# Optimization experiments

Measured on AMD Instinct MI355X. Metric: run time of the kernel, lower is better.

## Reference

```python
import jax, jax.numpy as jnp
import numpy as np

VQ_NUM = 3
EMB_NUM = 1024
COMMITMENT_WEIGHT = 1.0
# cumprod of [1, emb_num, emb_num] -> per-stage index bases
CUMPROD = [1, EMB_NUM, EMB_NUM * EMB_NUM]


def setup_inputs() -> dict:
    key = jax.random.key(0)
    k0, k1, k2, k3 = jax.random.split(key, 4)
    z = jax.random.normal(k0, (8, 4096, 512), dtype=jnp.float32)
    # linear_in: nn.Linear(in_ch=512, emb_ch=256, bias=False) -> weight [emb_ch, in_ch]
    W_in = jax.random.normal(k1, (VQ_NUM, 256, 512), dtype=jnp.float32) * 0.02
    # linear_out: nn.Linear(emb_ch=256, in_ch=512, bias=False) -> weight [in_ch, emb_ch]
    W_out = jax.random.normal(k2, (VQ_NUM, 512, 256), dtype=jnp.float32) * 0.02
    # one codebook per stage (share_residual_codebooks=False)
    codebooks = jax.random.normal(k3, (VQ_NUM, EMB_NUM, 256), dtype=jnp.float32) * 0.02
    return {"z": z, "W_in": W_in, "W_out": W_out, "codebooks": codebooks}


def reference(z, W_in, W_out, codebooks):
    sg = jax.lax.stop_gradient
    z_q = jnp.zeros_like(z)
    r = z
    loss = jnp.float32(0.0)
    index_sum = jnp.zeros(z.shape[:2], dtype=jnp.int64 if jax.config.jax_enable_x64 else jnp.int32)
    for i in range(VQ_NUM):
        # linear_in
        zi = jnp.einsum('bnc,ec->bne', r, W_in[i])  # [B,N,emb_ch]
        v = codebooks[i]  # [S, emb_ch]
        # squared L2 distance: ||z||^2 + ||v||^2 - 2 z.v
        dist = (jnp.sum(zi * zi, axis=-1, keepdims=True)
                + jnp.sum(v * v, axis=-1)
                - 2.0 * jnp.einsum('bne,se->bns', zi, v))  # [B,N,S]
        idx = jnp.argmin(dist, axis=-1)  # [B,N] int
        zq = v[idx]  # codebook lookup, [B,N,emb_ch]
        loss = loss + (COMMITMENT_WEIGHT * jnp.mean((sg(zq) - zi) ** 2)
                       + jnp.mean((zq - sg(zi)) ** 2))
        # straight-through estimator
        zq_ste = zi + sg(zq - zi)
        # linear_out
        r_q = jnp.einsum('bne,ce->bnc', zq_ste, W_out[i])  # [B,N,in_ch]
        index_sum = index_sum + idx.astype(index_sum.dtype) * CUMPROD[i]
        z_q = z_q + r_q
        r = z - sg(z_q)
    loss = loss / VQ_NUM + jnp.mean((z_q - z) ** 2)
    return z_q, index_sum, loss
```

## Files before the change

kernel.cpp:

```cpp
#include <hip/hip_runtime.h>

#define MTOK 32768
#define CIN  512
#define EMB  256
#define NCODE 1024
#define VQ   3
#define DELTA 2e-3f

typedef short s16x8 __attribute__((ext_vector_type(8)));
typedef float f32x4 __attribute__((ext_vector_type(4)));
typedef unsigned short u16;

static __device__ __forceinline__ u16 f2bf(float x) {
    unsigned int u = __float_as_uint(x);
    u += 0x7FFF + ((u >> 16) & 1);
    return (u16)(u >> 16);
}
static __device__ __forceinline__ float bf2f(u16 h) {
    return __uint_as_float(((unsigned int)h) << 16);
}

__global__ void init_k(double* loss_acc, int* cnt) {
    loss_acc[0] = 0.0;
    loss_acc[1] = 0.0;
    cnt[0] = 0; cnt[1] = 0; cnt[2] = 0;
}

__global__ __launch_bounds__(64) void prep_cb_k(const float* __restrict__ cbs,
                                                double* __restrict__ vnorm64,
                                                float* __restrict__ vnorm32,
                                                u16* __restrict__ cbh,
                                                u16* __restrict__ cbl) {
    int s = blockIdx.x;
    const float* row = cbs + (size_t)s * EMB;
    double acc = 0.0;
    for (int k = threadIdx.x; k < EMB; k += 64) {
        float v = row[k];
        double vd = (double)v; acc += vd * vd;
        u16 h = f2bf(v);
        u16 l = f2bf(v - bf2f(h));
        cbh[(size_t)s * EMB + k] = h;
        cbl[(size_t)s * EMB + k] = l;
    }
    #pragma unroll
    for (int off = 32; off > 0; off >>= 1) acc += __shfl_down(acc, off, 64);
    if (threadIdx.x == 0) { vnorm64[s] = acc; vnorm32[s] = (float)acc; }
}

__global__ __launch_bounds__(256) void prep_w_k(const float* __restrict__ W_in,
                                                u16* __restrict__ wh,
                                                u16* __restrict__ wl) {
    int i = blockIdx.x * 256 + threadIdx.x;
    float v = W_in[i];
    u16 h = f2bf(v);
    wh[i] = h;
    wl[i] = f2bf(v - bf2f(h));
}

__global__ __launch_bounds__(256) void prep_wt_k(const float* __restrict__ W_in,
                                                 float* __restrict__ WinT) {
    int i = blockIdx.x * 256 + threadIdx.x;
    int s = i / (EMB * CIN);
    int rem = i - s * (EMB * CIN);
    int e = rem / CIN;
    int k = rem - e * CIN;
    WinT[(size_t)s * CIN * EMB + (size_t)k * EMB + e] = W_in[i];
}

__global__ __launch_bounds__(256) void prep_T_k(const float* __restrict__ cbs,
                                                const float* __restrict__ Wout,
                                                float* __restrict__ T) {
    const int stage = blockIdx.z;
    const float* A = cbs  + (size_t)stage * NCODE * EMB;
    const float* B = Wout + (size_t)stage * CIN * EMB;
    float* C = T + (size_t)stage * NCODE * CIN;
    __shared__ float As[64][33];
    __shared__ float Bs[64][33];
    const int tid = threadIdx.x;
    const int ty = tid >> 4, tx = tid & 15;
    const int m0 = blockIdx.x * 64;
    const int n0 = blockIdx.y * 64;
    const int lrow = tid >> 5, lcol = tid & 31;
    double acc[4][4];
    #pragma unroll
    for (int i = 0; i < 4; ++i)
        #pragma unroll
        for (int j = 0; j < 4; ++j) acc[i][j] = 0.0;

    for (int k0 = 0; k0 < EMB; k0 += 32) {
        __syncthreads();
        #pragma unroll
        for (int t = 0; t < 8; ++t) {
            int r = lrow + 8 * t;
            As[r][lcol] = A[(size_t)(m0 + r) * EMB + k0 + lcol];
            Bs[r][lcol] = B[(size_t)(n0 + r) * EMB + k0 + lcol];
        }
        __syncthreads();
        #pragma unroll
        for (int k = 0; k < 32; ++k) {
            double a[4], b[4];
            #pragma unroll
            for (int i = 0; i < 4; ++i) a[i] = (double)As[ty * 4 + i][k];
            #pragma unroll
            for (int j = 0; j < 4; ++j) b[j] = (double)Bs[tx * 4 + j][k];
            #pragma unroll
            for (int i = 0; i < 4; ++i)
                #pragma unroll
                for (int j = 0; j < 4; ++j) acc[i][j] += a[i] * b[j];
        }
    }
    #pragma unroll
    for (int i = 0; i < 4; ++i) {
        float4 v = make_float4((float)acc[i][0], (float)acc[i][1],
                               (float)acc[i][2], (float)acc[i][3]);
        *reinterpret_cast<float4*>(&C[(size_t)(m0 + ty * 4 + i) * CIN + n0 + tx * 4]) = v;
    }
}

__global__ __launch_bounds__(256, 2) void zi_mfma_k(const float* __restrict__ z,
                                                    const float* __restrict__ zq,
                                                    const u16* __restrict__ wh,
                                                    const u16* __restrict__ wl,
                                                    float* __restrict__ zi,
                                                    double* __restrict__ loss_acc,
                                                    int stage0) {
    __shared__ __align__(16) u16 swh[2][16][520];
    __shared__ __align__(16) u16 swl[2][16][520];
    const int tid = threadIdx.x;
    const int w = tid >> 6;
    const int l = tid & 63;
    const int col = l & 15;
    const int g = l >> 4;
    const int mw = blockIdx.x * 64 + w * 16;
    const int sr = tid >> 4, sq = tid & 15;

    s16x8 ah[16], al[16];
    {
        const float* zr = z  + (size_t)(mw + col) * CIN + g * 8;
        const float* qr = zq + (size_t)(mw + col) * CIN + g * 8;
        #pragma unroll
        for (int kc = 0; kc < 16; ++kc) {
            float4 f0 = *reinterpret_cast<const float4*>(zr + kc * 32);
            float4 f1 = *reinterpret_cast<const float4*>(zr + kc * 32 + 4);
            float f[8] = {f0.x, f0.y, f0.z, f0.w, f1.x, f1.y, f1.z, f1.w};
            if (!stage0) {
                float4 q0 = *reinterpret_cast<const float4*>(qr + kc * 32);
                float4 q1 = *reinterpret_cast<const float4*>(qr + kc * 32 + 4);
                f[0] -= q0.x; f[1] -= q0.y; f[2] -= q0.z; f[3] -= q0.w;
                f[4] -= q1.x; f[5] -= q1.y; f[6] -= q1.z; f[7] -= q1.w;
            }
            #pragma unroll
            for (int j = 0; j < 8; ++j) {
                u16 h = f2bf(f[j]);
                u16 lo = f2bf(f[j] - bf2f(h));
                ah[kc][j] = (short)h; al[kc][j] = (short)lo;
            }
        }
    }

    const u16* gh = wh + (size_t)sr * CIN + sq * 8;
    const u16* gl = wl + (size_t)sr * CIN + sq * 8;
    uint4 h0, h1, h2, h3, l0, l1, l2, l3;
#define ZLOAD(NT) do { const u16* th = gh + (size_t)(NT) * (16 * CIN);                \
    const u16* tl = gl + (size_t)(NT) * (16 * CIN);                                   \
    h0 = *(const uint4*)(th);        h1 = *(const uint4*)(th + 128);                  \
    h2 = *(const uint4*)(th + 256);  h3 = *(const uint4*)(th + 384);                  \
    l0 = *(const uint4*)(tl);        l1 = *(const uint4*)(tl + 128);                  \
    l2 = *(const uint4*)(tl + 256);  l3 = *(const uint4*)(tl + 384); } while (0)
#define ZWRITE(P) do {                                                                \
    *(uint4*)&swh[P][sr][sq * 8]       = h0;  *(uint4*)&swh[P][sr][sq * 8 + 128] = h1;\
    *(uint4*)&swh[P][sr][sq * 8 + 256] = h2;  *(uint4*)&swh[P][sr][sq * 8 + 384] = h3;\
    *(uint4*)&swl[P][sr][sq * 8]       = l0;  *(uint4*)&swl[P][sr][sq * 8 + 128] = l1;\
    *(uint4*)&swl[P][sr][sq * 8 + 256] = l2;  *(uint4*)&swl[P][sr][sq * 8 + 384] = l3;\
    } while (0)
    ZLOAD(0); ZWRITE(0); ZLOAD(1);

    double zn = 0.0;
    for (int nt = 0; nt < 16; ++nt) {
        __syncthreads();
        const int p = nt & 1;
        if (nt + 1 < 16) ZWRITE((nt + 1) & 1);
        if (nt + 2 < 16) ZLOAD(nt + 2);
        f32x4 a0 = {0.f, 0.f, 0.f, 0.f};
        f32x4 a1 = {0.f, 0.f, 0.f, 0.f};
        f32x4 a2 = {0.f, 0.f, 0.f, 0.f};
        #pragma unroll
        for (int kc = 0; kc < 16; ++kc) {
            s16x8 Bh = *(const s16x8*)&swh[p][col][g * 8 + kc * 32];
            s16x8 Bl = *(const s16x8*)&swl[p][col][g * 8 + kc * 32];
            a0 = __builtin_amdgcn_mfma_f32_16x16x32_bf16(ah[kc], Bh, a0, 0, 0, 0);
            a1 = __builtin_amdgcn_mfma_f32_16x16x32_bf16(al[kc], Bh, a1, 0, 0, 0);
            a2 = __builtin_amdgcn_mfma_f32_16x16x32_bf16(ah[kc], Bl, a2, 0, 0, 0);
        }
        #pragma unroll
        for (int r = 0; r < 4; ++r) {
            float v = a0[r] + a1[r] + a2[r];
            zi[(size_t)(mw + g * 4 + r) * EMB + nt * 16 + col] = v;
            zn += (double)v * (double)v;
        }
    }
#undef ZLOAD
#undef ZWRITE
    #pragma unroll
    for (int off = 32; off > 0; off >>= 1) zn += __shfl_down(zn, off, 64);
    if (l == 0) atomicAdd(loss_acc, zn);
}

__global__ __launch_bounds__(256, 2) void pref_k(const float* __restrict__ zi,
                                                 const u16* __restrict__ cbh,
                                                 const u16* __restrict__ cbl,
                                                 const float* __restrict__ vnorm32,
                                                 int* __restrict__ idx,
                                                 int* __restrict__ idx_sum,
                                                 float* __restrict__ mind,
                                                 int* __restrict__ flagged,
                                                 int* __restrict__ cnt,
                                                 int* __restrict__ cand2,
                                                 double* __restrict__ loss_acc,
                                                 int stage0, int cumprod) {
    __shared__ __align__(16) u16 sbh[2][16][264];
    __shared__ __align__(16) u16 sbl[2][16][264];
    __shared__ double loss_s[16];
    const int tid = threadIdx.x;
    const int w = tid >> 6;
    const int l = tid & 63;
    const int col = l & 15;
    const int g = l >> 4;
    const int mw = blockIdx.x * 64 + w * 16;
    const int sr = tid >> 4, sq = tid & 15;

    s16x8 ah[8], al[8];
    {
        const float* zr = zi + (size_t)(mw + col) * EMB + g * 8;
        #pragma unroll
        for (int kc = 0; kc < 8; ++kc) {
            float4 f0 = *reinterpret_cast<const float4*>(zr + kc * 32);
            float4 f1 = *reinterpret_cast<const float4*>(zr + kc * 32 + 4);
            float f[8] = {f0.x, f0.y, f0.z, f0.w, f1.x, f1.y, f1.z, f1.w};
            #pragma unroll
            for (int j = 0; j < 8; ++j) {
                u16 h = f2bf(f[j]);
                u16 lo = f2bf(f[j] - bf2f(h));
                ah[kc][j] = (short)h;
                al[kc][j] = (short)lo;
            }
        }
    }

    float b1[4] = {1e30f, 1e30f, 1e30f, 1e30f};
    float b2[4] = {1e30f, 1e30f, 1e30f, 1e30f};
    float b3[4] = {1e30f, 1e30f, 1e30f, 1e30f};
    int   i1[4] = {0, 0, 0, 0};
    int   i2[4] = {0, 0, 0, 0};

    const u16* gh = cbh + (size_t)sr * EMB + sq * 8;
    const u16* gl = cbl + (size_t)sr * EMB + sq * 8;
    uint4 h0, h1, l0, l1;
#define PLOAD(CT) do { const u16* th = gh + (size_t)(CT) * (16 * EMB);                \
    const u16* tl = gl + (size_t)(CT) * (16 * EMB);                                   \
    h0 = *(const uint4*)(th);  h1 = *(const uint4*)(th + 128);                        \
    l0 = *(const uint4*)(tl);  l1 = *(const uint4*)(tl + 128); } while (0)
#define PWRITE(P) do {                                                                \
    *(uint4*)&sbh[P][sr][sq * 8] = h0;  *(uint4*)&sbh[P][sr][sq * 8 + 128] = h1;      \
    *(uint4*)&sbl[P][sr][sq * 8] = l0;  *(uint4*)&sbl[P][sr][sq * 8 + 128] = l1;      \
    } while (0)
    PLOAD(0); PWRITE(0); PLOAD(1);

    for (int ct = 0; ct < 64; ++ct) {
        __syncthreads();
        const int p = ct & 1;
        if (ct + 1 < 64) PWRITE((ct + 1) & 1);
        if (ct + 2 < 64) PLOAD(ct + 2);
        const float vn = vnorm32[ct * 16 + col];
        f32x4 a0 = {0.f, 0.f, 0.f, 0.f};
        f32x4 a1 = {0.f, 0.f, 0.f, 0.f};
        f32x4 a2 = {0.f, 0.f, 0.f, 0.f};
        #pragma unroll
        for (int kc = 0; kc < 8; ++kc) {
            s16x8 Bh = *(const s16x8*)&sbh[p][col][g * 8 + kc * 32];
            s16x8 Bl = *(const s16x8*)&sbl[p][col][g * 8 + kc * 32];
            a0 = __builtin_amdgcn_mfma_f32_16x16x32_bf16(ah[kc], Bh, a0, 0, 0, 0);
            a1 = __builtin_amdgcn_mfma_f32_16x16x32_bf16(al[kc], Bh, a1, 0, 0, 0);
            a2 = __builtin_amdgcn_mfma_f32_16x16x32_bf16(ah[kc], Bl, a2, 0, 0, 0);
        }
        #pragma unroll
        for (int r = 0; r < 4; ++r) {
            float sc = vn - 2.f * (a0[r] + a1[r] + a2[r]);
            int c = ct * 16 + col;
            if (sc < b1[r]) { b3[r] = b2[r]; b2[r] = b1[r]; i2[r] = i1[r]; b1[r] = sc; i1[r] = c; }
            else if (sc < b2[r]) { b3[r] = b2[r]; b2[r] = sc; i2[r] = c; }
            else b3[r] = fminf(b3[r], sc);
        }
    }
#undef PLOAD
#undef PWRITE

    #pragma unroll
    for (int off = 1; off < 16; off <<= 1) {
        #pragma unroll
        for (int r = 0; r < 4; ++r) {
            float c1 = __shfl_xor(b1[r], off, 64);
            int   j1 = __shfl_xor(i1[r], off, 64);
            float c2 = __shfl_xor(b2[r], off, 64);
            int   j2 = __shfl_xor(i2[r], off, 64);
            float c3 = __shfl_xor(b3[r], off, 64);
            float nb1, nb2, nb3; int ni1, ni2;
            if (c1 < b1[r] || (c1 == b1[r] && j1 < i1[r])) {
                nb1 = c1; ni1 = j1;
                if (b1[r] < c2 || (b1[r] == c2 && i1[r] < j2)) {
                    nb2 = b1[r]; ni2 = i1[r]; nb3 = fminf(b2[r], c2);
                } else {
                    nb2 = c2; ni2 = j2; nb3 = fminf(b1[r], c3);
                }
            } else {
                nb1 = b1[r]; ni1 = i1[r];
                if (c1 < b2[r] || (c1 == b2[r] && j1 < i2[r])) {
                    nb2 = c1; ni2 = j1; nb3 = fminf(b2[r], c2);
                } else {
                    nb2 = b2[r]; ni2 = i2[r]; nb3 = fminf(c1, b3[r]);
                }
            }
            b1[r] = nb1; b2[r] = nb2; b3[r] = nb3; i1[r] = ni1; i2[r] = ni2;
        }
    }
    if (col == 0) {
        double lsum = 0.0;
        #pragma unroll
        for (int r = 0; r < 4; ++r) {
            int m = mw + g * 4 + r;
            idx[m] = i1[r];
            if (stage0) idx_sum[m] = i1[r];
            else        idx_sum[m] += i1[r] * cumprod;
            mind[m] = b1[r];
            lsum += (double)b1[r];
            if (b2[r] - b1[r] < DELTA) {
                int slot = atomicAdd(cnt, 1);
                int full = (b3[r] - b1[r] < DELTA) ? 1 : 0;
                flagged[slot] = (m << 1) | full;
                cand2[m] = i2[r];
            }
        }
        loss_s[w * 4 + g] = lsum;
    }
    __syncthreads();
    if (tid == 0) {
        double s = 0.0;
        #pragma unroll
        for (int q = 0; q < 16; ++q) s += loss_s[q];
        atomicAdd(loss_acc, s);
    }
}

__global__ __launch_bounds__(256) void rescan_k(const float* __restrict__ z,
                                                const float* __restrict__ zqv,
                                                const float* __restrict__ WinT,
                                                const float* __restrict__ cb,
                                                const double* __restrict__ vnorm64,
                                                const int* __restrict__ flagged,
                                                const int* __restrict__ cnt,
                                                const int* __restrict__ cand2,
                                                int* __restrict__ idx,
                                                int* __restrict__ idx_sum,
                                                float* __restrict__ mind,
                                                double* __restrict__ loss_acc,
                                                int cumprod, int stage0) {
    __shared__ double r64[8][CIN];
    __shared__ int mArr[8], fArr[8], cAArr[8], cBArr[8];
    __shared__ double sredS[4];
    __shared__ int iredS[4];
    double* zi_l = &r64[0][0];
    const int tid = threadIdx.x;
    const int w = tid >> 6, l = tid & 63;
    const int n = *cnt;

    for (int jb = blockIdx.x; jb * 8 < n; jb += gridDim.x) {
        const int nt = min(8, n - jb * 8);
        __syncthreads();
        if (tid < nt) {
            int fm = flagged[jb * 8 + tid];
            int m = fm >> 1;
            mArr[tid] = m; fArr[tid] = fm & 1;
            cAArr[tid] = idx[m]; cBArr[tid] = cand2[m];
        }
        __syncthreads();
        for (int t = 0; t < nt; ++t) {
            const int m = mArr[t];
            #pragma unroll
            for (int h = 0; h < 2; ++h) {
                int k = tid + h * 256;
                float rv = z[(size_t)m * CIN + k];
                if (!stage0) rv -= zqv[(size_t)m * CIN + k];
                r64[t][k] = (double)rv;
            }
        }
        __syncthreads();
        double acc[8] = {0, 0, 0, 0, 0, 0, 0, 0};
        #pragma unroll 4
        for (int k = 0; k < CIN; ++k) {
            double wv = (double)WinT[(size_t)k * EMB + tid];
            #pragma unroll
            for (int t = 0; t < 8; ++t) acc[t] += r64[t][k] * wv;
        }
        __syncthreads();
        #pragma unroll
        for (int t = 0; t < 8; ++t) zi_l[t * 256 + tid] = acc[t];
        __syncthreads();

        for (int t = w; t < nt; t += 4) {
            if (fArr[t]) continue;
            const int cA = cAArr[t], cB = cBArr[t], m = mArr[t];
            const double* zt = zi_l + t * 256;
            float4 vA = *(const float4*)(cb + (size_t)cA * EMB + 4 * l);
            float4 vB = *(const float4*)(cb + (size_t)cB * EMB + 4 * l);
            double z0 = zt[4 * l], z1 = zt[4 * l + 1];
            double z2 = zt[4 * l + 2], z3 = zt[4 * l + 3];
            double sA = z0 * (double)vA.x + z1 * (double)vA.y
                      + z2 * (double)vA.z + z3 * (double)vA.w;
            double sB = z0 * (double)vB.x + z1 * (double)vB.y
                      + z2 * (double)vB.z + z3 * (double)vB.w;
            #pragma unroll
            for (int off = 1; off < 64; off <<= 1) {
                sA += __shfl_xor(sA, off, 64);
                sB += __shfl_xor(sB, off, 64);
            }
            if (l == 0) {
                double dA = vnorm64[cA] - 2.0 * sA;
                double dB = vnorm64[cB] - 2.0 * sB;
                int bi; double best;
                if (dB < dA || (dB == dA && cB < cA)) { bi = cB; best = dB; }
                else                                   { bi = cA; best = dA; }
                int oldI = idx[m];
                if (bi != oldI) { idx[m] = bi; idx_sum[m] += (bi - oldI) * cumprod; }
                atomicAdd(loss_acc, best - (double)mind[m]);
                mind[m] = (float)best;
            }
        }

        for (int t = 0; t < nt; ++t) {
            if (!fArr[t]) continue;
            const int m = mArr[t];
            const double* zt = zi_l + t * 256;
            double bs = 1e300; int bc = 0;
            #pragma unroll
            for (int r = 0; r < 4; ++r) {
                const int c = (w << 8) + (r << 6) + l;
                const float* row = cb + (size_t)c * EMB;
                double s0 = 0, s1 = 0, s2 = 0, s3 = 0;
                for (int e = 0; e < EMB; e += 4) {
                    s0 += zt[e]     * (double)row[e];
                    s1 += zt[e + 1] * (double)row[e + 1];
                    s2 += zt[e + 2] * (double)row[e + 2];
                    s3 += zt[e + 3] * (double)row[e + 3];
                }
                double sc = vnorm64[c] - 2.0 * ((s0 + s1) + (s2 + s3));
                if (sc < bs) { bs = sc; bc = c; }
            }
            #pragma unroll
            for (int off = 1; off < 64; off <<= 1) {
                double ob = __shfl_xor(bs, off, 64);
                int    oc = __shfl_xor(bc, off, 64);
                if (ob < bs || (ob == bs && oc < bc)) { bs = ob; bc = oc; }
            }
            if (l == 0) { sredS[w] = bs; iredS[w] = bc; }
            __syncthreads();
            if (tid == 0) {
                double best = sredS[0]; int bi = iredS[0];
                for (int q = 1; q < 4; ++q)
                    if (sredS[q] < best || (sredS[q] == best && iredS[q] < bi)) {
                        best = sredS[q]; bi = iredS[q];
                    }
                int oldI = idx[m];
                if (bi != oldI) { idx[m] = bi; idx_sum[m] += (bi - oldI) * cumprod; }
                atomicAdd(loss_acc, best - (double)mind[m]);
                mind[m] = (float)best;
            }
            __syncthreads();
        }
    }
}

__global__ __launch_bounds__(256) void gather_k(const float* __restrict__ T,
                                                const int* __restrict__ idx,
                                                const float* __restrict__ z,
                                                float* __restrict__ zq,
                                                int stage0, int last,
                                                double* __restrict__ loss_acc) {
    __shared__ double red[256];
    int m = blockIdx.x * 16 + (threadIdx.x >> 4);
    int q = threadIdx.x & 15;
    const float* src = T + (size_t)idx[m] * CIN;
    float* dst = zq + (size_t)m * CIN;
    double s = 0.0;
    #pragma unroll
    for (int it = 0; it < 8; ++it) {
        int off = it * 64 + q * 4;
        float4 t = *reinterpret_cast<const float4*>(src + off);
        if (!stage0) {
            float4 o = *reinterpret_cast<const float4*>(dst + off);
            t.x += o.x; t.y += o.y; t.z += o.z; t.w += o.w;
        }
        *reinterpret_cast<float4*>(dst + off) = t;
        if (last) {
            float4 zv = *reinterpret_cast<const float4*>(z + (size_t)m * CIN + off);
            double d0 = (double)zv.x - (double)t.x;
            double d1 = (double)zv.y - (double)t.y;
            double d2 = (double)zv.z - (double)t.z;
            double d3 = (double)zv.w - (double)t.w;
            s += d0 * d0 + d1 * d1 + d2 * d2 + d3 * d3;
        }
    }
    if (last) {
        red[threadIdx.x] = s;
        __syncthreads();
        for (int off = 128; off > 0; off >>= 1) {
            if (threadIdx.x < off) red[threadIdx.x] += red[threadIdx.x + off];
            __syncthreads();
        }
        if (threadIdx.x == 0) atomicAdd(loss_acc + 1, red[0]);
    }
}

__global__ void final_k(const int* __restrict__ idx_sum,
                        const double* __restrict__ loss_acc,
                        float* __restrict__ out) {
    int i = blockIdx.x * blockDim.x + threadIdx.x;
    if (i < MTOK) out[MTOK * CIN + i] = (float)idx_sum[i];
    if (i == 0) {
        double loss = 2.0 * loss_acc[0] / (3.0 * (double)MTOK * (double)EMB)
                    + loss_acc[1] / ((double)MTOK * (double)CIN);
        out[MTOK * CIN + MTOK] = (float)loss;
    }
}

extern "C" void kernel_launch(void* const* d_in, const int* in_sizes, int n_in,
                              void* d_out, int out_size, void* d_ws, size_t ws_size,
                              hipStream_t stream) {
    const float* z     = (const float*)d_in[0];
    const float* W_in  = (const float*)d_in[1];
    const float* W_out = (const float*)d_in[2];
    const float* cbs   = (const float*)d_in[3];
    float* out = (float*)d_out;
    char* ws = (char*)d_ws;

    double* vnorm64  = (double*)ws;
    double* loss_acc = (double*)(ws + 24576);
    float*  vnorm32  = (float*)(ws + 24592);
    int*    cnt      = (int*)(ws + 36880);
    u16*    cbh      = (u16*)(ws + 36896);
    u16*    cbl      = (u16*)(ws + 1609760);
    u16*    wh       = (u16*)(ws + 3182624);
    u16*    wl       = (u16*)(ws + 3969056);
    float*  WinT     = (float*)(ws + 4755488);
    float*  T        = (float*)(ws + 6328352);
    float*  zi       = (float*)(ws + 12619808);
    char*   p        = ws + 12619808 + (size_t)MTOK * EMB * 4;
    int*    idx      = (int*)p;
    int*    idx_sum  = (int*)(p + 131072);
    int*    flagged  = (int*)(p + 262144);
    float*  mind     = (float*)(p + 393216);
    int*    cand2    = (int*)(p + 524288);

    float* zq = out;

    init_k<<<dim3(1), dim3(1), 0, stream>>>(loss_acc, cnt);
    prep_cb_k<<<dim3(VQ * NCODE), dim3(64), 0, stream>>>(cbs, vnorm64, vnorm32, cbh, cbl);
    prep_w_k<<<dim3(VQ * EMB * CIN / 256), dim3(256), 0, stream>>>(W_in, wh, wl);
    prep_wt_k<<<dim3(VQ * EMB * CIN / 256), dim3(256), 0, stream>>>(W_in, WinT);
    prep_T_k<<<dim3(NCODE / 64, CIN / 64, VQ), dim3(256), 0, stream>>>(cbs, W_out, T);

    const int cumprod[VQ] = {1, 1024, 1024 * 1024};
    for (int i = 0; i < VQ; ++i) {
        const float* cb = cbs + (size_t)i * NCODE * EMB;
        zi_mfma_k<<<dim3(MTOK / 64), dim3(256), 0, stream>>>(
            z, zq, wh + (size_t)i * EMB * CIN, wl + (size_t)i * EMB * CIN,
            zi, loss_acc, i == 0 ? 1 : 0);
        pref_k<<<dim3(MTOK / 64), dim3(256), 0, stream>>>(
            zi, cbh + (size_t)i * NCODE * EMB, cbl + (size_t)i * NCODE * EMB,
            vnorm32 + i * NCODE, idx, idx_sum, mind, flagged, cnt + i, cand2,
            loss_acc, i == 0 ? 1 : 0, cumprod[i]);
        rescan_k<<<dim3(256), dim3(256), 0, stream>>>(
            z, zq, WinT + (size_t)i * EMB * CIN, cb, vnorm64 + i * NCODE,
            flagged, cnt + i, cand2, idx, idx_sum, mind, loss_acc, cumprod[i],
            i == 0 ? 1 : 0);
        gather_k<<<dim3(MTOK / 16), dim3(256), 0, stream>>>(
            T + (size_t)i * NCODE * CIN, idx, z, zq, i == 0 ? 1 : 0,
            i == VQ - 1 ? 1 : 0, loss_acc);
    }
    final_k<<<dim3(MTOK / 256), dim3(256), 0, stream>>>(idx_sum, loss_acc, out);
}
```

Baseline: 930.4 us.

## Split ambiguous-token rescan into separate pair and full-codebook kernels

The prefilter now writes ambiguous tokens to two lists. Tokens with only two close candidates go to a pair-rescan kernel, and tokens needing a full codebook search go to a new fullscan kernel that handles one token per block. The full scan now gives each lane a slice of the embedding and reads codebook rows coalesced as float4, instead of having each thread loop over a whole row. The pair kernel's grid doubles and no longer carries a serial, sync-heavy full-scan loop. This costs an extra kernel launch per stage, and the fullscan kernel recomputes the double-precision projection once per token.

```diff
diff --git a/kernel.cpp b/kernel.cpp
--- a/kernel.cpp
+++ b/kernel.cpp
@@ -23,7 +23,8 @@
 __global__ void init_k(double* loss_acc, int* cnt) {
     loss_acc[0] = 0.0;
     loss_acc[1] = 0.0;
-    cnt[0] = 0; cnt[1] = 0; cnt[2] = 0;
+    #pragma unroll
+    for (int i = 0; i < 8; ++i) cnt[i] = 0;
 }
 
 __global__ __launch_bounds__(64) void prep_cb_k(const float* __restrict__ cbs,
@@ -215,6 +216,8 @@
                                                  float* __restrict__ mind,
                                                  int* __restrict__ flagged,
                                                  int* __restrict__ cnt,
+                                                 int* __restrict__ fullList,
+                                                 int* __restrict__ cntF,
                                                  int* __restrict__ cand2,
                                                  double* __restrict__ loss_acc,
                                                  int stage0, int cumprod) {
@@ -334,10 +337,14 @@
             mind[m] = b1[r];
             lsum += (double)b1[r];
             if (b2[r] - b1[r] < DELTA) {
-                int slot = atomicAdd(cnt, 1);
-                int full = (b3[r] - b1[r] < DELTA) ? 1 : 0;
-                flagged[slot] = (m << 1) | full;
-                cand2[m] = i2[r];
+                if (b3[r] - b1[r] < DELTA) {
+                    int slot = atomicAdd(cntF, 1);
+                    fullList[slot] = m;
+                } else {
+                    int slot = atomicAdd(cnt, 1);
+                    flagged[slot] = m;
+                    cand2[m] = i2[r];
+                }
             }
         }
         loss_s[w * 4 + g] = lsum;
@@ -351,23 +358,21 @@
     }
 }
 
-__global__ __launch_bounds__(256) void rescan_k(const float* __restrict__ z,
-                                                const float* __restrict__ zqv,
-                                                const float* __restrict__ WinT,
-                                                const float* __restrict__ cb,
-                                                const double* __restrict__ vnorm64,
-                                                const int* __restrict__ flagged,
-                                                const int* __restrict__ cnt,
-                                                const int* __restrict__ cand2,
-                                                int* __restrict__ idx,
-                                                int* __restrict__ idx_sum,
-                                                float* __restrict__ mind,
-                                                double* __restrict__ loss_acc,
-                                                int cumprod, int stage0) {
+__global__ __launch_bounds__(256) void rescan_pair_k(const float* __restrict__ z,
+                                                     const float* __restrict__ zqv,
+                                                     const float* __restrict__ WinT,
+                                                     const float* __restrict__ cb,
+                                                     const double* __restrict__ vnorm64,
+                                                     const int* __restrict__ flagged,
+                                                     const int* __restrict__ cnt,
+                                                     const int* __restrict__ cand2,
+                                                     int* __restrict__ idx,
+                                                     int* __restrict__ idx_sum,
+                                                     float* __restrict__ mind,
+                                                     double* __restrict__ loss_acc,
+                                                     int cumprod, int stage0) {
     __shared__ double r64[8][CIN];
-    __shared__ int mArr[8], fArr[8], cAArr[8], cBArr[8];
-    __shared__ double sredS[4];
-    __shared__ int iredS[4];
+    __shared__ int mArr[8], cAArr[8], cBArr[8];
     double* zi_l = &r64[0][0];
     const int tid = threadIdx.x;
     const int w = tid >> 6, l = tid & 63;
@@ -377,9 +382,8 @@
         const int nt = min(8, n - jb * 8);
         __syncthreads();
         if (tid < nt) {
-            int fm = flagged[jb * 8 + tid];
-            int m = fm >> 1;
-            mArr[tid] = m; fArr[tid] = fm & 1;
+            int m = flagged[jb * 8 + tid];
+            mArr[tid] = m;
             cAArr[tid] = idx[m]; cBArr[tid] = cand2[m];
         }
         __syncthreads();
@@ -407,7 +411,6 @@
         __syncthreads();
 
         for (int t = w; t < nt; t += 4) {
-            if (fArr[t]) continue;
             const int cA = cAArr[t], cB = cBArr[t], m = mArr[t];
             const double* zt = zi_l + t * 256;
             float4 vA = *(const float4*)(cb + (size_t)cA * EMB + 4 * l);
@@ -435,46 +438,72 @@
                 mind[m] = (float)best;
             }
         }
-
-        for (int t = 0; t < nt; ++t) {
-            if (!fArr[t]) continue;
-            const int m = mArr[t];
-            const double* zt = zi_l + t * 256;
-            double bs = 1e300; int bc = 0;
-            #pragma unroll
-            for (int r = 0; r < 4; ++r) {
-                const int c = (w << 8) + (r << 6) + l;
-                const float* row = cb + (size_t)c * EMB;
-                double s0 = 0, s1 = 0, s2 = 0, s3 = 0;
-                for (int e = 0; e < EMB; e += 4) {
-                    s0 += zt[e]     * (double)row[e];
-                    s1 += zt[e + 1] * (double)row[e + 1];
-                    s2 += zt[e + 2] * (double)row[e + 2];
-                    s3 += zt[e + 3] * (double)row[e + 3];
+    }
+}
+
+__global__ __launch_bounds__(256) void fullscan_k(const float* __restrict__ z,
+                                                  const float* __restrict__ zqv,
+                                                  const float* __restrict__ WinT,
+                                                  const float* __restrict__ cb,
+                                                  const double* __restrict__ vnorm64,
+                                                  const int* __restrict__ fullList,
+                                                  const int* __restrict__ cntF,
+                                                  int* __restrict__ idx,
+                                                  int* __restrict__ idx_sum,
+                                                  float* __restrict__ mind,
+                                                  double* __restrict__ loss_acc,
+                                                  int cumprod, int stage0) {
+    __shared__ double r64[CIN];
+    __shared__ double zi64[EMB];
+    __shared__ double sredS[4];
+    __shared__ int iredS[4];
+    const int tid = threadIdx.x;
+    const int w = tid >> 6, l = tid & 63;
+    const int n = *cntF;
+
+    for (int j = blockIdx.x; j < n; j += gridDim.x) {
+        const int m = fullList[j];
+        __syncthreads();
+        #pragma unroll
+        for (int h = 0; h < 2; ++h) {
+            int k = tid + h * 256;
+            float rv = z[(size_t)m * CIN + k];
+            if (!stage0) rv -= zqv[(size_t)m * CIN + k];
+            r64[k] = (double)rv;
+        }
+        __syncthreads();
+        {
+            double acc = 0.0;
+            #pragma unroll 8
+            for (int k = 0; k < CIN; ++k)
+                acc += r64[k] * (double)WinT[(size_t)k * EMB + tid];
+            zi64[tid] = acc;
+        }
+        __syncthreads();
+        const double z0 = zi64[4 * l], z1 = zi64[4 * l + 1];
+        const double z2 = zi64[4 * l + 2], z3 = zi64[4 * l + 3];
+        double bs = 1e300; int bc = 0;
+        for (int c = w * 256; c < w * 256 + 256; ++c) {
+            float4 v = *(const float4*)(cb + (size_t)c * EMB + 4 * l);
+            double s = z0 * (double)v.x + z1 * (double)v.y
+                     + z2 * (double)v.z + z3 * (double)v.w;
+            #pragma unroll
+            for (int off = 1; off < 64; off <<= 1) s += __shfl_xor(s, off, 64);
+            double sc = vnorm64[c] - 2.0 * s;
+            if (sc < bs) { bs = sc; bc = c; }
+        }
+        if (l == 0) { sredS[w] = bs; iredS[w] = bc; }
+        __syncthreads();
+        if (tid == 0) {
+            double best = sredS[0]; int bi = iredS[0];
+            for (int q = 1; q < 4; ++q)
+                if (sredS[q] < best || (sredS[q] == best && iredS[q] < bi)) {
+                    best = sredS[q]; bi = iredS[q];
                 }
-                double sc = vnorm64[c] - 2.0 * ((s0 + s1) + (s2 + s3));
-                if (sc < bs) { bs = sc; bc = c; }
-            }
-            #pragma unroll
-            for (int off = 1; off < 64; off <<= 1) {
-                double ob = __shfl_xor(bs, off, 64);
-                int    oc = __shfl_xor(bc, off, 64);
-                if (ob < bs || (ob == bs && oc < bc)) { bs = ob; bc = oc; }
-            }
-            if (l == 0) { sredS[w] = bs; iredS[w] = bc; }
-            __syncthreads();
-            if (tid == 0) {
-                double best = sredS[0]; int bi = iredS[0];
-                for (int q = 1; q < 4; ++q)
-                    if (sredS[q] < best || (sredS[q] == best && iredS[q] < bi)) {
-                        best = sredS[q]; bi = iredS[q];
-                    }
-                int oldI = idx[m];
-                if (bi != oldI) { idx[m] = bi; idx_sum[m] += (bi - oldI) * cumprod; }
-                atomicAdd(loss_acc, best - (double)mind[m]);
-                mind[m] = (float)best;
-            }
-            __syncthreads();
+            int oldI = idx[m];
+            if (bi != oldI) { idx[m] = bi; idx_sum[m] += (bi - oldI) * cumprod; }
+            atomicAdd(loss_acc, best - (double)mind[m]);
+            mind[m] = (float)best;
         }
     }
 }
@@ -544,21 +573,22 @@
 
     double* vnorm64  = (double*)ws;
     double* loss_acc = (double*)(ws + 24576);
-    float*  vnorm32  = (float*)(ws + 24592);
-    int*    cnt      = (int*)(ws + 36880);
-    u16*    cbh      = (u16*)(ws + 36896);
-    u16*    cbl      = (u16*)(ws + 1609760);
-    u16*    wh       = (u16*)(ws + 3182624);
-    u16*    wl       = (u16*)(ws + 3969056);
-    float*  WinT     = (float*)(ws + 4755488);
-    float*  T        = (float*)(ws + 6328352);
-    float*  zi       = (float*)(ws + 12619808);
-    char*   p        = ws + 12619808 + (size_t)MTOK * EMB * 4;
+    int*    cnt      = (int*)(ws + 24592);
+    float*  vnorm32  = (float*)(ws + 24624);
+    u16*    cbh      = (u16*)(ws + 36912);
+    u16*    cbl      = (u16*)(ws + 1609776);
+    u16*    wh       = (u16*)(ws + 3182640);
+    u16*    wl       = (u16*)(ws + 3969072);
+    float*  WinT     = (float*)(ws + 4755504);
+    float*  T        = (float*)(ws + 6328368);
+    float*  zi       = (float*)(ws + 12619824);
+    char*   p        = ws + 46174256;
     int*    idx      = (int*)p;
     int*    idx_sum  = (int*)(p + 131072);
     int*    flagged  = (int*)(p + 262144);
     float*  mind     = (float*)(p + 393216);
     int*    cand2    = (int*)(p + 524288);
+    int*    fullList = (int*)(p + 655360);
 
     float* zq = out;
 
@@ -576,11 +606,15 @@
             zi, loss_acc, i == 0 ? 1 : 0);
         pref_k<<<dim3(MTOK / 64), dim3(256), 0, stream>>>(
             zi, cbh + (size_t)i * NCODE * EMB, cbl + (size_t)i * NCODE * EMB,
-            vnorm32 + i * NCODE, idx, idx_sum, mind, flagged, cnt + i, cand2,
-            loss_acc, i == 0 ? 1 : 0, cumprod[i]);
-        rescan_k<<<dim3(256), dim3(256), 0, stream>>>(
+            vnorm32 + i * NCODE, idx, idx_sum, mind, flagged, cnt + i,
+            fullList, cnt + 3 + i, cand2, loss_acc, i == 0 ? 1 : 0, cumprod[i]);
+        rescan_pair_k<<<dim3(512), dim3(256), 0, stream>>>(
             z, zq, WinT + (size_t)i * EMB * CIN, cb, vnorm64 + i * NCODE,
             flagged, cnt + i, cand2, idx, idx_sum, mind, loss_acc, cumprod[i],
+            i == 0 ? 1 : 0);
+        fullscan_k<<<dim3(256), dim3(256), 0, stream>>>(
+            z, zq, WinT + (size_t)i * EMB * CIN, cb, vnorm64 + i * NCODE,
+            fullList, cnt + 3 + i, idx, idx_sum, mind, loss_acc, cumprod[i],
             i == 0 ? 1 : 0);
         gather_k<<<dim3(MTOK / 16), dim3(256), 0, stream>>>(
             T + (size_t)i * NCODE * CIN, idx, z, zq, i == 0 ? 1 : 0,
```

Measured after the change: 1.188 ms. 27.7% more time.
